# Performance work log

Measured on AMD Instinct MI355X. Metric: run time of the kernel, lower is better.

## Reference

```python
import jax, jax.numpy as jnp
import numpy as np

HIDDEN = 512
HEAD = 64
SEQ = 2048
CHUNK = 256
GAMMA = 0.96875
SCALE_BASE = 512.0


def _xpos(x, downscale):
    # x: [B, L, hd]; XPOS with offset=0 (scale rows == length, no trimming needed)
    B, L, hd = x.shape
    half = hd // 2
    scale_vec = (jnp.arange(0, hd, 2, dtype=jnp.float32) + 0.4 * hd) / (1.4 * hd)  # [half]
    power = jnp.arange(L, dtype=jnp.float32) / SCALE_BASE                          # [L]
    scale = scale_vec[None, :] ** power[:, None]                                   # [L, half]
    inv_freq = 1.0 / (10000.0 ** (jnp.arange(half, dtype=jnp.float32) / half))
    sinusoid = jnp.arange(L, dtype=jnp.float32)[:, None] * inv_freq[None, :]       # [L, half]
    sin, cos = jnp.sin(sinusoid), jnp.cos(sinusoid)
    if downscale:
        scale = 1.0 / scale
    # duplicate_interleave: repeat each column twice -> [L, hd]
    sin_f = jnp.repeat(sin * scale, 2, axis=-1)
    cos_f = jnp.repeat(cos * scale, 2, axis=-1)
    x1 = x[:, :, 0::2]
    x2 = x[:, :, 1::2]
    rot = jnp.stack((-x2, x1), axis=-1).reshape(B, L, hd)  # rotate_every_two
    return x * cos_f + rot * sin_f


def _D_parallel():
    # D[i, j] = gamma^|i-j| if j < (i//chunk + 1)*chunk else 0 (block-causal with in-chunk lookahead)
    i = jnp.arange(SEQ)[:, None]
    j = jnp.arange(SEQ)[None, :]
    j_max = (i // CHUNK + 1) * CHUNK
    decay = GAMMA ** jnp.abs(i - j).astype(jnp.float32)
    return jnp.where(j < j_max, decay, 0.0)  # gamma>0 so no NaNs to scrub


def setup_inputs() -> dict:
    key = jax.random.key(0)
    k1, k2, k3, k4 = jax.random.split(key, 4)
    X = jax.random.normal(k1, (8, SEQ, HIDDEN), dtype=jnp.float32)
    W_Q = jax.random.normal(k2, (HIDDEN, HEAD), dtype=jnp.float32) / HIDDEN
    W_K = jax.random.normal(k3, (HIDDEN, HEAD), dtype=jnp.float32) / HIDDEN
    W_V = jax.random.normal(k4, (HIDDEN, HEAD), dtype=jnp.float32) / HIDDEN
    return {"X": X, "W_Q": W_Q, "W_K": W_K, "W_V": W_V}


def reference(X, W_Q, W_K, W_V):
    Q = _xpos(X @ W_Q, downscale=False)   # [B, S, H]
    K = _xpos(X @ W_K, downscale=True)    # [B, S, H]
    V = X @ W_V                           # [B, S, V]
    D = _D_parallel()                     # [S, S]
    scores = jnp.einsum('bqh,bkh->bqk', Q, K) * D[None]
    return jnp.einsum('bqk,bkv->bqv', scores, V)
```

## Files before the change

kernel.cpp:

```cpp
#include <hip/hip_runtime.h>
#include <hip/hip_bf16.h>


typedef __attribute__((ext_vector_type(8))) short short8;
typedef __attribute__((ext_vector_type(4))) float floatx4;

#define LOG2GAMMA (-0.04580350f)

static __device__ __forceinline__ unsigned short f2bf(float f) {
    __hip_bfloat16 h = __float2bfloat16(f);
    return *reinterpret_cast<unsigned short*>(&h);
}

__global__ __launch_bounds__(256) void prep_kernel(
    const float* __restrict__ Wq, const float* __restrict__ Wk,
    const float* __restrict__ Wv,
    __hip_bfloat16* __restrict__ Wt, float* __restrict__ tabs)
{
    int idx = blockIdx.x * 256 + threadIdx.x;
    const int WT_N = 192 * 512;
    if (idx < WT_N) {
        int n = idx >> 9, k = idx & 511;
        int m = n >> 6, c = n & 63;
        const float* W = (m == 0) ? Wq : ((m == 1) ? Wk : Wv);
        Wt[idx] = __float2bfloat16(W[k * 64 + c]);
    } else {
        int t2 = idx - WT_N;
        if (t2 < 4 * 2048 * 32) {
            int tab = t2 >> 16;
            int rem = t2 & 65535;
            int pos = rem >> 5;
            int t   = rem & 31;
            float inv_freq = powf(10000.0f, -(float)t / 32.0f);
            float sinus = (float)pos * inv_freq;
            float s = sinf(sinus), c = cosf(sinus);
            float sv = (2.0f * (float)t + 0.4f * 64.0f) / (1.4f * 64.0f);
            float power = (float)pos / 512.0f;
            float scl = powf(sv, (tab >= 2) ? -power : power);
            tabs[t2] = ((tab & 1) == 0) ? c * scl : s * scl;
        }
    }
}

__global__ __launch_bounds__(256, 2) void proj_kernel(
    const float* __restrict__ X, const __hip_bfloat16* __restrict__ Wt,
    const float* __restrict__ tabs,
    __hip_bfloat16* __restrict__ Qb, __hip_bfloat16* __restrict__ Kb,
    __hip_bfloat16* __restrict__ Vt)
{
    __shared__ __hip_bfloat16 lx[32][136];
    __shared__ __hip_bfloat16 lw[192][136];

    int tid = threadIdx.x;
    int r0 = blockIdx.x * 32;
    int w = tid >> 6, lane = tid & 63, quad = lane >> 4, l15 = lane & 15;
    int rh = w & 1, nh = w >> 1;

    floatx4 acc[6];
#pragma unroll
    for (int t = 0; t < 6; t++) acc[t] = (floatx4){0.f, 0.f, 0.f, 0.f};

    for (int kb = 0; kb < 4; kb++) {
#pragma unroll
        for (int u = 0; u < 4; u++) {
            int f = u * 256 + tid;
            int row = f >> 5, c = f & 31;
            float4 v = *(const float4*)(X + (r0 + row) * 512 + kb * 128 + c * 4);
            ushort4 pk;
            pk.x = f2bf(v.x); pk.y = f2bf(v.y); pk.z = f2bf(v.z); pk.w = f2bf(v.w);
            *(ushort4*)&lx[row][c * 4] = pk;
        }
#pragma unroll
        for (int u = 0; u < 12; u++) {
            int f = u * 256 + tid;
            int row = f >> 4, c = f & 15;
            uint4 v = *(const uint4*)(Wt + row * 512 + kb * 128 + c * 8);
            *(uint4*)&lw[row][c * 8] = v;
        }
        __syncthreads();
#pragma unroll
        for (int ks = 0; ks < 4; ks++) {
            short8 a = *(const short8*)&lx[rh * 16 + l15][ks * 32 + quad * 8];
#pragma unroll
            for (int t = 0; t < 6; t++) {
                short8 bfr = *(const short8*)&lw[(nh * 6 + t) * 16 + l15][ks * 32 + quad * 8];
                acc[t] = __builtin_amdgcn_mfma_f32_16x16x32_bf16(a, bfr, acc[t], 0, 0, 0);
            }
        }
        __syncthreads();
    }

    int b0 = r0 >> 11, n0 = r0 & 2047;
    int rbase = r0 + rh * 16 + quad * 4;

    __hip_bfloat16* lvt = &lx[0][0];
    if (nh == 1) {
#pragma unroll
        for (int tl = 2; tl < 6; tl++) {
            int ch = (tl - 2) * 16 + l15;
#pragma unroll
            for (int rg = 0; rg < 4; rg++)
                lvt[ch * 40 + rh * 16 + quad * 4 + rg] = __float2bfloat16(acc[tl][rg]);
        }
    }
    __syncthreads();

#pragma unroll
    for (int tl = 0; tl < 6; tl++) {
        int t = nh * 6 + tl;
        if (t >= 8) break;
#pragma unroll
        for (int rg = 0; rg < 4; rg++) {
            int r = rbase + rg;
            int b = r >> 11, n = r & 2047;
            float val = acc[tl][rg];
            float prt = __shfl_xor(val, 1, 64);
            if (t < 4) {
                int ch = t * 16 + l15;
                int tt = ch >> 1;
                float co = tabs[n * 32 + tt];
                float si = tabs[65536 + n * 32 + tt];
                float o = (l15 & 1) ? (val * co + prt * si) : (val * co - prt * si);
                Qb[(b * 2048 + n) * 64 + ch] = __float2bfloat16(o);
            } else {
                int ch = (t - 4) * 16 + l15;
                int tt = ch >> 1;
                float co = tabs[131072 + n * 32 + tt];
                float si = tabs[196608 + n * 32 + tt];
                float o = (l15 & 1) ? (val * co + prt * si) : (val * co - prt * si);
                Kb[(b * 2048 + n) * 64 + ch] = __float2bfloat16(o);
            }
        }
    }

    {
        int row = tid >> 2, c = tid & 3;
        uint4 v = *(const uint4*)&lvt[row * 40 + c * 8];
        *(uint4*)(Vt + ((size_t)(b0 * 64 + row)) * 2048 + n0 + c * 8) = v;
    }
}

__global__ __launch_bounds__(256, 3) void attn_kernel(
    const __hip_bfloat16* __restrict__ Qb, const __hip_bfloat16* __restrict__ Kb,
    const __hip_bfloat16* __restrict__ Vt, float* __restrict__ out)
{
    __shared__ __hip_bfloat16 lk[256][72];
    __shared__ __hip_bfloat16 lp[32][264];

    int tid = threadIdx.x;
    int b = blockIdx.x >> 6, qt = blockIdx.x & 63;
    int q0 = qt * 32, qc = q0 >> 8;
    int w = tid >> 6, lane = tid & 63, quad = lane >> 4, l15 = lane & 15;
    int rh = w & 1, ph = w >> 1;

    short8 qf[2];
#pragma unroll
    for (int kk = 0; kk < 2; kk++)
        qf[kk] = *(const short8*)(Qb + ((size_t)(b * 2048 + q0 + rh * 16 + l15)) * 64 + kk * 32 + quad * 8);

    const __hip_bfloat16* vbase = Vt + (size_t)b * 64 * 2048;

    floatx4 o[2];
    o[0] = (floatx4){0.f, 0.f, 0.f, 0.f};
    o[1] = (floatx4){0.f, 0.f, 0.f, 0.f};

    int kc0 = (qc >= 3) ? (qc - 3) : 0;
    for (int kc = kc0; kc <= qc; kc++) {
        int kbase = kc * 256;
#pragma unroll
        for (int u = 0; u < 8; u++) {
            int f = u * 256 + tid;
            int row = f >> 3, c = f & 7;
            *(uint4*)&lk[row][c * 8] =
                *(const uint4*)(Kb + ((size_t)(b * 2048 + kbase + row)) * 64 + c * 8);
        }
        __syncthreads();

        floatx4 s[8];
#pragma unroll
        for (int t = 0; t < 8; t++) s[t] = (floatx4){0.f, 0.f, 0.f, 0.f};
#pragma unroll
        for (int t = 0; t < 8; t++) {
#pragma unroll
            for (int kk = 0; kk < 2; kk++) {
                short8 bfr = *(const short8*)&lk[(ph * 8 + t) * 16 + l15][kk * 32 + quad * 8];
                s[t] = __builtin_amdgcn_mfma_f32_16x16x32_bf16(qf[kk], bfr, s[t], 0, 0, 0);
            }
        }

        int i0 = q0 + rh * 16 + quad * 4;
#pragma unroll
        for (int t = 0; t < 8; t++) {
            int j = kbase + (ph * 8 + t) * 16 + l15;
#pragma unroll
            for (int rg = 0; rg < 4; rg++) {
                int d = i0 + rg - j; d = (d < 0) ? -d : d;
                float p = s[t][rg] * exp2f(LOG2GAMMA * (float)d);
                lp[rh * 16 + quad * 4 + rg][(ph * 8 + t) * 16 + l15] = __float2bfloat16(p);
            }
        }
        __syncthreads();

#pragma unroll
        for (int ks = 0; ks < 8; ks++) {
            short8 a = *(const short8*)&lp[rh * 16 + l15][ks * 32 + quad * 8];
#pragma unroll
            for (int tt = 0; tt < 2; tt++) {
                int t2 = ph * 2 + tt;
                short8 bfr = *(const short8*)(vbase + ((size_t)(t2 * 16 + l15)) * 2048
                                              + kbase + ks * 32 + quad * 8);
                o[tt] = __builtin_amdgcn_mfma_f32_16x16x32_bf16(a, bfr, o[tt], 0, 0, 0);
            }
        }
    }

    int rbase = b * 2048 + q0 + rh * 16 + quad * 4;
#pragma unroll
    for (int tt = 0; tt < 2; tt++)
#pragma unroll
        for (int rg = 0; rg < 4; rg++)
            out[((size_t)(rbase + rg)) * 64 + (ph * 2 + tt) * 16 + l15] = o[tt][rg];
}

extern "C" void kernel_launch(void* const* d_in, const int* in_sizes, int n_in,
                              void* d_out, int out_size, void* d_ws, size_t ws_size,
                              hipStream_t stream) {
    const float* X  = (const float*)d_in[0];
    const float* Wq = (const float*)d_in[1];
    const float* Wk = (const float*)d_in[2];
    const float* Wv = (const float*)d_in[3];
    float* out = (float*)d_out;

    char* ws = (char*)d_ws;
    __hip_bfloat16* Wt   = (__hip_bfloat16*)(ws);
    float*          tabs = (float*)(ws + 196608);
    __hip_bfloat16* Qb   = (__hip_bfloat16*)(ws + 1245184);
    __hip_bfloat16* Kb   = (__hip_bfloat16*)(ws + 3342336);
    __hip_bfloat16* Vt   = (__hip_bfloat16*)(ws + 5439488);

    prep_kernel<<<1408, 256, 0, stream>>>(Wq, Wk, Wv, Wt, tabs);
    proj_kernel<<<512, 256, 0, stream>>>(X, Wt, tabs, Qb, Kb, Vt);
    attn_kernel<<<512, 256, 0, stream>>>(Qb, Kb, Vt, out);
}
```

Before: 125.7 us.

## Store W, Q, K, V in MFMA fragment order and split key chunks across waves

```diff
diff --git a/kernel.cpp b/kernel.cpp
--- a/kernel.cpp
+++ b/kernel.cpp
@@ -12,20 +12,27 @@
     return *reinterpret_cast<unsigned short*>(&h);
 }
 
+
 __global__ __launch_bounds__(256) void prep_kernel(
     const float* __restrict__ Wq, const float* __restrict__ Wk,
     const float* __restrict__ Wv,
-    __hip_bfloat16* __restrict__ Wt, float* __restrict__ tabs)
+    __hip_bfloat16* __restrict__ Wfrag, float* __restrict__ tabs)
 {
     int idx = blockIdx.x * 256 + threadIdx.x;
-    const int WT_N = 192 * 512;
-    if (idx < WT_N) {
-        int n = idx >> 9, k = idx & 511;
+    const int WF_N = 192 * 512;
+    if (idx < WF_N) {
+        int j    = idx & 7;
+        int n15  = (idx >> 3) & 15;
+        int quad = (idx >> 7) & 3;
+        int kkg  = (idx >> 9) & 15;
+        int tile = idx >> 13;
+        int n = tile * 16 + n15;
+        int k = kkg * 32 + quad * 8 + j;
         int m = n >> 6, c = n & 63;
         const float* W = (m == 0) ? Wq : ((m == 1) ? Wk : Wv);
-        Wt[idx] = __float2bfloat16(W[k * 64 + c]);
+        Wfrag[idx] = __float2bfloat16(W[k * 64 + c]);
     } else {
-        int t2 = idx - WT_N;
+        int t2 = idx - WF_N;
         if (t2 < 4 * 2048 * 32) {
             int tab = t2 >> 16;
             int rem = t2 & 65535;
@@ -42,14 +49,13 @@
     }
 }
 
-__global__ __launch_bounds__(256, 2) void proj_kernel(
-    const float* __restrict__ X, const __hip_bfloat16* __restrict__ Wt,
+__global__ __launch_bounds__(256, 4) void proj_kernel(
+    const float* __restrict__ X, const __hip_bfloat16* __restrict__ Wfrag,
     const float* __restrict__ tabs,
-    __hip_bfloat16* __restrict__ Qb, __hip_bfloat16* __restrict__ Kb,
-    __hip_bfloat16* __restrict__ Vt)
+    __hip_bfloat16* __restrict__ Qfrag, __hip_bfloat16* __restrict__ Kfrag,
+    __hip_bfloat16* __restrict__ Vfrag)
 {
-    __shared__ __hip_bfloat16 lx[32][136];
-    __shared__ __hip_bfloat16 lw[192][136];
+    __shared__ __hip_bfloat16 smem[7168];
 
     int tid = threadIdx.x;
     int r0 = blockIdx.x * 32;
@@ -68,158 +74,155 @@
             float4 v = *(const float4*)(X + (r0 + row) * 512 + kb * 128 + c * 4);
             ushort4 pk;
             pk.x = f2bf(v.x); pk.y = f2bf(v.y); pk.z = f2bf(v.z); pk.w = f2bf(v.w);
-            *(ushort4*)&lx[row][c * 4] = pk;
-        }
-#pragma unroll
-        for (int u = 0; u < 12; u++) {
-            int f = u * 256 + tid;
-            int row = f >> 4, c = f & 15;
-            uint4 v = *(const uint4*)(Wt + row * 512 + kb * 128 + c * 8);
-            *(uint4*)&lw[row][c * 8] = v;
+            *(ushort4*)&smem[row * 136 + c * 4] = pk;
         }
         __syncthreads();
 #pragma unroll
         for (int ks = 0; ks < 4; ks++) {
-            short8 a = *(const short8*)&lx[rh * 16 + l15][ks * 32 + quad * 8];
+            short8 a = *(const short8*)&smem[(rh * 16 + l15) * 136 + ks * 32 + quad * 8];
+            int kkg = kb * 4 + ks;
 #pragma unroll
             for (int t = 0; t < 6; t++) {
-                short8 bfr = *(const short8*)&lw[(nh * 6 + t) * 16 + l15][ks * 32 + quad * 8];
+                int tile = nh * 6 + t;
+                short8 bfr = *(const short8*)(Wfrag + ((tile * 16 + kkg) * 64 + lane) * 8);
                 acc[t] = __builtin_amdgcn_mfma_f32_16x16x32_bf16(a, bfr, acc[t], 0, 0, 0);
             }
         }
         __syncthreads();
     }
 
-    int b0 = r0 >> 11, n0 = r0 & 2047;
-    int rbase = r0 + rh * 16 + quad * 4;
-
-    __hip_bfloat16* lvt = &lx[0][0];
-    if (nh == 1) {
-#pragma unroll
-        for (int tl = 2; tl < 6; tl++) {
-            int ch = (tl - 2) * 16 + l15;
-#pragma unroll
-            for (int rg = 0; rg < 4; rg++)
-                lvt[ch * 40 + rh * 16 + quad * 4 + rg] = __float2bfloat16(acc[tl][rg]);
-        }
-    }
-    __syncthreads();
+    __hip_bfloat16* bufQ = smem;
+    __hip_bfloat16* bufK = smem + 2304;
+    __hip_bfloat16* bufV = smem + 4608;
+    int b = r0 >> 11, n0 = r0 & 2047;
+    int rrow = rh * 16 + quad * 4;
 
 #pragma unroll
     for (int tl = 0; tl < 6; tl++) {
         int t = nh * 6 + tl;
-        if (t >= 8) break;
 #pragma unroll
         for (int rg = 0; rg < 4; rg++) {
-            int r = rbase + rg;
-            int b = r >> 11, n = r & 2047;
+            int row = rrow + rg;
+            int n = n0 + row;
             float val = acc[tl][rg];
             float prt = __shfl_xor(val, 1, 64);
             if (t < 4) {
-                int ch = t * 16 + l15;
-                int tt = ch >> 1;
+                int ch = t * 16 + l15, tt = ch >> 1;
                 float co = tabs[n * 32 + tt];
                 float si = tabs[65536 + n * 32 + tt];
                 float o = (l15 & 1) ? (val * co + prt * si) : (val * co - prt * si);
-                Qb[(b * 2048 + n) * 64 + ch] = __float2bfloat16(o);
-            } else {
-                int ch = (t - 4) * 16 + l15;
-                int tt = ch >> 1;
+                bufQ[row * 72 + ch] = __float2bfloat16(o);
+            } else if (t < 8) {
+                int ch = (t - 4) * 16 + l15, tt = ch >> 1;
                 float co = tabs[131072 + n * 32 + tt];
                 float si = tabs[196608 + n * 32 + tt];
                 float o = (l15 & 1) ? (val * co + prt * si) : (val * co - prt * si);
-                Kb[(b * 2048 + n) * 64 + ch] = __float2bfloat16(o);
-            }
-        }
-    }
+                bufK[row * 72 + ch] = __float2bfloat16(o);
+            } else {
+                int ch = (t - 8) * 16 + l15;
+                bufV[ch * 40 + row] = __float2bfloat16(val);
+            }
+        }
+    }
+    __syncthreads();
 
     {
-        int row = tid >> 2, c = tid & 3;
-        uint4 v = *(const uint4*)&lvt[row * 40 + c * 8];
-        *(uint4*)(Vt + ((size_t)(b0 * 64 + row)) * 2048 + n0 + c * 8) = v;
+        int tile2 = tid >> 7, kk = (tid >> 6) & 1, ln = tid & 63;
+        int q2 = ln >> 4, m15 = ln & 15;
+        size_t qkbase = ((((size_t)b * 128 + (n0 >> 4) + tile2) * 2 + kk) * 64 + ln) * 8;
+        uint4 vq = *(const uint4*)&bufQ[(tile2 * 16 + m15) * 72 + kk * 32 + q2 * 8];
+        *(uint4*)(Qfrag + qkbase) = vq;
+        uint4 vk = *(const uint4*)&bufK[(tile2 * 16 + m15) * 72 + kk * 32 + q2 * 8];
+        *(uint4*)(Kfrag + qkbase) = vk;
+        int t2 = tid >> 6;
+        uint4 vv = *(const uint4*)&bufV[(t2 * 16 + m15) * 40 + q2 * 8];
+        *(uint4*)(Vfrag + ((((size_t)b * 64 + (n0 >> 5)) * 4 + t2) * 64 + ln) * 8) = vv;
     }
 }
 
 __global__ __launch_bounds__(256, 3) void attn_kernel(
-    const __hip_bfloat16* __restrict__ Qb, const __hip_bfloat16* __restrict__ Kb,
-    const __hip_bfloat16* __restrict__ Vt, float* __restrict__ out)
+    const __hip_bfloat16* __restrict__ Qfrag, const __hip_bfloat16* __restrict__ Kfrag,
+    const __hip_bfloat16* __restrict__ Vfrag, float* __restrict__ out)
 {
-    __shared__ __hip_bfloat16 lk[256][72];
-    __shared__ __hip_bfloat16 lp[32][264];
+    __shared__ __hip_bfloat16 lp[4][16 * 264];
 
     int tid = threadIdx.x;
     int b = blockIdx.x >> 6, qt = blockIdx.x & 63;
     int q0 = qt * 32, qc = q0 >> 8;
     int w = tid >> 6, lane = tid & 63, quad = lane >> 4, l15 = lane & 15;
-    int rh = w & 1, ph = w >> 1;
+    int qh = w >> 1, h = w & 1;
+    int qt16 = (q0 >> 4) + qh;
 
     short8 qf[2];
 #pragma unroll
     for (int kk = 0; kk < 2; kk++)
-        qf[kk] = *(const short8*)(Qb + ((size_t)(b * 2048 + q0 + rh * 16 + l15)) * 64 + kk * 32 + quad * 8);
-
-    const __hip_bfloat16* vbase = Vt + (size_t)b * 64 * 2048;
-
-    floatx4 o[2];
-    o[0] = (floatx4){0.f, 0.f, 0.f, 0.f};
-    o[1] = (floatx4){0.f, 0.f, 0.f, 0.f};
+        qf[kk] = *(const short8*)(Qfrag + ((((size_t)b * 128 + qt16) * 2 + kk) * 64 + lane) * 8);
+
+    __hip_bfloat16* P = &lp[w][0];
+
+    floatx4 o[4];
+#pragma unroll
+    for (int t = 0; t < 4; t++) o[t] = (floatx4){0.f, 0.f, 0.f, 0.f};
 
     int kc0 = (qc >= 3) ? (qc - 3) : 0;
-    for (int kc = kc0; kc <= qc; kc++) {
+    for (int kc = kc0 + h; kc <= qc; kc += 2) {
+        floatx4 s[16];
+#pragma unroll
+        for (int t = 0; t < 16; t++) s[t] = (floatx4){0.f, 0.f, 0.f, 0.f};
+#pragma unroll
+        for (int t = 0; t < 16; t++) {
+#pragma unroll
+            for (int kk = 0; kk < 2; kk++) {
+                short8 bfr = *(const short8*)(Kfrag +
+                    ((((size_t)b * 128 + kc * 16 + t) * 2 + kk) * 64 + lane) * 8);
+                s[t] = __builtin_amdgcn_mfma_f32_16x16x32_bf16(qf[kk], bfr, s[t], 0, 0, 0);
+            }
+        }
+
+        int i0 = q0 + qh * 16 + quad * 4;
         int kbase = kc * 256;
 #pragma unroll
-        for (int u = 0; u < 8; u++) {
-            int f = u * 256 + tid;
-            int row = f >> 3, c = f & 7;
-            *(uint4*)&lk[row][c * 8] =
-                *(const uint4*)(Kb + ((size_t)(b * 2048 + kbase + row)) * 64 + c * 8);
-        }
-        __syncthreads();
-
-        floatx4 s[8];
-#pragma unroll
-        for (int t = 0; t < 8; t++) s[t] = (floatx4){0.f, 0.f, 0.f, 0.f};
-#pragma unroll
-        for (int t = 0; t < 8; t++) {
-#pragma unroll
-            for (int kk = 0; kk < 2; kk++) {
-                short8 bfr = *(const short8*)&lk[(ph * 8 + t) * 16 + l15][kk * 32 + quad * 8];
-                s[t] = __builtin_amdgcn_mfma_f32_16x16x32_bf16(qf[kk], bfr, s[t], 0, 0, 0);
-            }
-        }
-
-        int i0 = q0 + rh * 16 + quad * 4;
-#pragma unroll
-        for (int t = 0; t < 8; t++) {
-            int j = kbase + (ph * 8 + t) * 16 + l15;
+        for (int t = 0; t < 16; t++) {
+            int j = kbase + t * 16 + l15;
 #pragma unroll
             for (int rg = 0; rg < 4; rg++) {
                 int d = i0 + rg - j; d = (d < 0) ? -d : d;
                 float p = s[t][rg] * exp2f(LOG2GAMMA * (float)d);
-                lp[rh * 16 + quad * 4 + rg][(ph * 8 + t) * 16 + l15] = __float2bfloat16(p);
-            }
-        }
-        __syncthreads();
+                P[(quad * 4 + rg) * 264 + t * 16 + l15] = __float2bfloat16(p);
+            }
+        }
 
 #pragma unroll
         for (int ks = 0; ks < 8; ks++) {
-            short8 a = *(const short8*)&lp[rh * 16 + l15][ks * 32 + quad * 8];
-#pragma unroll
-            for (int tt = 0; tt < 2; tt++) {
-                int t2 = ph * 2 + tt;
-                short8 bfr = *(const short8*)(vbase + ((size_t)(t2 * 16 + l15)) * 2048
-                                              + kbase + ks * 32 + quad * 8);
-                o[tt] = __builtin_amdgcn_mfma_f32_16x16x32_bf16(a, bfr, o[tt], 0, 0, 0);
-            }
-        }
-    }
-
-    int rbase = b * 2048 + q0 + rh * 16 + quad * 4;
-#pragma unroll
-    for (int tt = 0; tt < 2; tt++)
-#pragma unroll
-        for (int rg = 0; rg < 4; rg++)
-            out[((size_t)(rbase + rg)) * 64 + (ph * 2 + tt) * 16 + l15] = o[tt][rg];
+            short8 a = *(const short8*)&P[l15 * 264 + ks * 32 + quad * 8];
+#pragma unroll
+            for (int t2 = 0; t2 < 4; t2++) {
+                short8 bfr = *(const short8*)(Vfrag +
+                    ((((size_t)b * 64 + kc * 8 + ks) * 4 + t2) * 64 + lane) * 8);
+                o[t2] = __builtin_amdgcn_mfma_f32_16x16x32_bf16(a, bfr, o[t2], 0, 0, 0);
+            }
+        }
+    }
+
+    float* mine = (float*)&lp[w][0];
+    float* part = (float*)&lp[w ^ 1][0];
+    if (h == 1) {
+#pragma unroll
+        for (int t2 = 0; t2 < 4; t2++)
+#pragma unroll
+            for (int rg = 0; rg < 4; rg++)
+                mine[(quad * 4 + rg) * 64 + t2 * 16 + l15] = o[t2][rg];
+    }
+    __syncthreads();
+    if (h == 0) {
+        int rbase = b * 2048 + q0 + qh * 16 + quad * 4;
+#pragma unroll
+        for (int t2 = 0; t2 < 4; t2++)
+#pragma unroll
+            for (int rg = 0; rg < 4; rg++)
+                out[(size_t)(rbase + rg) * 64 + t2 * 16 + l15] =
+                    o[t2][rg] + part[(quad * 4 + rg) * 64 + t2 * 16 + l15];
+    }
 }
 
 extern "C" void kernel_launch(void* const* d_in, const int* in_sizes, int n_in,
@@ -232,13 +235,13 @@
     float* out = (float*)d_out;
 
     char* ws = (char*)d_ws;
-    __hip_bfloat16* Wt   = (__hip_bfloat16*)(ws);
-    float*          tabs = (float*)(ws + 196608);
-    __hip_bfloat16* Qb   = (__hip_bfloat16*)(ws + 1245184);
-    __hip_bfloat16* Kb   = (__hip_bfloat16*)(ws + 3342336);
-    __hip_bfloat16* Vt   = (__hip_bfloat16*)(ws + 5439488);
-
-    prep_kernel<<<1408, 256, 0, stream>>>(Wq, Wk, Wv, Wt, tabs);
-    proj_kernel<<<512, 256, 0, stream>>>(X, Wt, tabs, Qb, Kb, Vt);
-    attn_kernel<<<512, 256, 0, stream>>>(Qb, Kb, Vt, out);
-}
+    __hip_bfloat16* Wfrag = (__hip_bfloat16*)(ws);
+    float*          tabs  = (float*)(ws + 196608);
+    __hip_bfloat16* Qfrag = (__hip_bfloat16*)(ws + 1245184);
+    __hip_bfloat16* Kfrag = (__hip_bfloat16*)(ws + 3342336);
+    __hip_bfloat16* Vfrag = (__hip_bfloat16*)(ws + 5439488);
+
+    prep_kernel<<<1408, 256, 0, stream>>>(Wq, Wk, Wv, Wfrag, tabs);
+    proj_kernel<<<512, 256, 0, stream>>>(X, Wfrag, tabs, Qfrag, Kfrag, Vfrag);
+    attn_kernel<<<512, 256, 0, stream>>>(Qfrag, Kfrag, Vfrag, out);
+}
```

New measurement: 127.9 us. Within noise of the previous version (+1.7%).
